# Optimization experiments

Measured on AMD Instinct MI355X. Metric: run time of the kernel, lower is better.

The kernel has to match this reference:

```python
import jax, jax.numpy as jnp
import numpy as np


def setup_inputs() -> dict:
    key = jax.random.key(0)
    kx, kw, kb = jax.random.split(key, 3)
    x = jax.random.normal(kx, (32, 256, 64, 64), dtype=jnp.float32)
    # Conv2d(in=2, out=1, kernel=7) weights, OIHW layout
    W = jax.random.normal(kw, (1, 2, 7, 7), dtype=jnp.float32) * 0.1
    b = jax.random.normal(kb, (1,), dtype=jnp.float32) * 0.1
    return {"x": x, "W": W, "b": b}


def reference(x, W, b):
    # Channel-wise max and mean pooling -> [B, 1, H, W] each
    maxpool = jnp.max(x, axis=1, keepdims=True)
    avgpool = jnp.mean(x, axis=1, keepdims=True)
    pool = jnp.concatenate([maxpool, avgpool], axis=1)  # [B, 2, H, W]
    # 7x7 conv, stride 1, padding 3 (SAME), NCHW / OIHW
    samap = jax.lax.conv_general_dilated(
        pool, W,
        window_strides=(1, 1),
        padding=[(3, 3), (3, 3)],
        dimension_numbers=("NCHW", "OIHW", "NCHW"),
    ) + b[None, :, None, None]
    samap = jax.nn.sigmoid(samap)  # [B, 1, H, W]
    return x * samap
```

## Files before the change

### kernel.cpp

```cpp
#include <hip/hip_runtime.h>
#include <math.h>

constexpr int B_  = 32;
constexpr int C_  = 256;
constexpr int H_  = 64;
constexpr int W_  = 64;
constexpr int HW_ = H_ * W_;
constexpr size_t CHW_ = (size_t)C_ * HW_;

__global__ __launch_bounds__(256) void pool_kernel(const float* __restrict__ x,
                                                   float* __restrict__ pool) {
    const int blk = blockIdx.x;
    const int b   = blk >> 6;
    const int h   = blk & 63;
    const int tid = threadIdx.x;
    const int wg  = tid & 15;
    const int cg  = tid >> 4;

    const float* base = x + (size_t)b * CHW_ + (size_t)(cg * 16) * HW_ + h * W_ + wg * 4;
    float4 v  = *(const float4*)base;
    float4 mx = v, sm = v;
#pragma unroll
    for (int c = 1; c < 16; ++c) {
        float4 u = *(const float4*)(base + (size_t)c * HW_);
        mx.x = fmaxf(mx.x, u.x); mx.y = fmaxf(mx.y, u.y);
        mx.z = fmaxf(mx.z, u.z); mx.w = fmaxf(mx.w, u.w);
        sm.x += u.x; sm.y += u.y; sm.z += u.z; sm.w += u.w;
    }

    __shared__ float4 lmax[16][16];
    __shared__ float4 lsum[16][16];
    lmax[cg][wg] = mx;
    lsum[cg][wg] = sm;
    __syncthreads();

    if (tid < 16) {
        const int w = tid;
        float4 M = lmax[0][w], S = lsum[0][w];
#pragma unroll
        for (int g = 1; g < 16; ++g) {
            float4 m2 = lmax[g][w], s2 = lsum[g][w];
            M.x = fmaxf(M.x, m2.x); M.y = fmaxf(M.y, m2.y);
            M.z = fmaxf(M.z, m2.z); M.w = fmaxf(M.w, m2.w);
            S.x += s2.x; S.y += s2.y; S.z += s2.z; S.w += s2.w;
        }
        const float inv = 1.0f / 256.0f;
        float4 A = make_float4(S.x * inv, S.y * inv, S.z * inv, S.w * inv);
        float* pm = pool + (size_t)b * 2 * HW_ + h * W_ + w * 4;
        *(float4*)pm          = M;
        *(float4*)(pm + HW_)  = A;
    }
}

__global__ __launch_bounds__(256) void conv_kernel(const float* __restrict__ pool,
                                                   const float* __restrict__ Wp,
                                                   const float* __restrict__ bp,
                                                   float* __restrict__ samap) {
    __shared__ float sw[98];
    const int tid = threadIdx.x;
    if (tid < 98) sw[tid] = Wp[tid];
    __syncthreads();

    const int t  = blockIdx.x * 256 + tid;
    const int b  = t >> 12;
    const int hw = t & 4095;
    const int h  = hw >> 6;
    const int w  = hw & 63;

    const float* pb = pool + (size_t)b * 2 * HW_;
    float acc = bp[0];
#pragma unroll
    for (int i = 0; i < 2; ++i) {
        const float* pc = pb + i * HW_;
        const float* wc = sw + i * 49;
#pragma unroll
        for (int kh = 0; kh < 7; ++kh) {
            const int hh = h + kh - 3;
            if (hh < 0 || hh >= H_) continue;
#pragma unroll
            for (int kw = 0; kw < 7; ++kw) {
                const int ww = w + kw - 3;
                if (ww < 0 || ww >= W_) continue;
                acc = fmaf(pc[hh * W_ + ww], wc[kh * 7 + kw], acc);
            }
        }
    }
    samap[t] = 1.0f / (1.0f + expf(-acc));
}

__global__ __launch_bounds__(256) void scale_kernel(const float* __restrict__ x,
                                                    const float* __restrict__ samap,
                                                    float* __restrict__ out) {
    const int t = blockIdx.x * 256 + threadIdx.x;
    const size_t o = (size_t)t * 4;
    const int b  = (int)(o >> 20);
    const int hw = (int)(o & 4095);
    float4 xv = *(const float4*)(x + o);
    float4 sv = *(const float4*)(samap + b * HW_ + hw);
    float4 ov = make_float4(xv.x * sv.x, xv.y * sv.y, xv.z * sv.z, xv.w * sv.w);
    *(float4*)(out + o) = ov;
}

extern "C" void kernel_launch(void* const* d_in, const int* in_sizes, int n_in,
                              void* d_out, int out_size, void* d_ws, size_t ws_size,
                              hipStream_t stream) {
    const float* x  = (const float*)d_in[0];
    const float* Wp = (const float*)d_in[1];
    const float* bp = (const float*)d_in[2];
    float* out = (float*)d_out;

    float* pool  = (float*)d_ws;
    float* samap = pool + (size_t)B_ * 2 * HW_;

    pool_kernel<<<B_ * H_, 256, 0, stream>>>(x, pool);
    conv_kernel<<<(B_ * HW_) / 256, 256, 0, stream>>>(pool, Wp, bp, samap);
    scale_kernel<<<(B_ * (int)CHW_) / (4 * 256), 256, 0, stream>>>(x, samap, out);
}
```

Measured before the change: 264.1 us.

## Fuse conv and scale into one row-wise kernel with nontemporal stores

Merges the 7x7 conv+sigmoid kernel and the broadcast-scale kernel into one kernel per (batch, row). Each block stages the 7 pool rows in shared memory, computes 64 sigmoid values with 64 threads, then scales all 256 channels of that row and writes the output with nontemporal stores. This removes one launch and the samap round trip through global memory. In exchange, 3/4 of the threads sit idle during the conv phase and the block synchronizes before the big streaming phase.

```diff
diff --git a/kernel.cpp b/kernel.cpp
--- a/kernel.cpp
+++ b/kernel.cpp
@@ -7,6 +7,8 @@
 constexpr int W_  = 64;
 constexpr int HW_ = H_ * W_;
 constexpr size_t CHW_ = (size_t)C_ * HW_;
+
+typedef float v4f __attribute__((ext_vector_type(4)));
 
 __global__ __launch_bounds__(256) void pool_kernel(const float* __restrict__ x,
                                                    float* __restrict__ pool) {
@@ -52,53 +54,66 @@
     }
 }
 
-__global__ __launch_bounds__(256) void conv_kernel(const float* __restrict__ pool,
-                                                   const float* __restrict__ Wp,
-                                                   const float* __restrict__ bp,
-                                                   float* __restrict__ samap) {
+__global__ __launch_bounds__(256) void conv_scale_kernel(const float* __restrict__ x,
+                                                         const float* __restrict__ pool,
+                                                         const float* __restrict__ Wp,
+                                                         const float* __restrict__ bp,
+                                                         float* __restrict__ out) {
+    const int blk = blockIdx.x;
+    const int b   = blk >> 6;
+    const int h   = blk & 63;
+    const int tid = threadIdx.x;
+
     __shared__ float sw[98];
-    const int tid = threadIdx.x;
+    __shared__ float spool[2][7][64];
+    __shared__ float ssa[64];
+
     if (tid < 98) sw[tid] = Wp[tid];
+#pragma unroll
+    for (int idx = tid; idx < 896; idx += 256) {
+        const int plane = idx / 448;
+        const int rem   = idx - plane * 448;
+        const int r     = rem >> 6;
+        const int w     = rem & 63;
+        const int hh    = h + r - 3;
+        spool[plane][r][w] = (hh >= 0 && hh < H_)
+            ? pool[((size_t)b * 2 + plane) * HW_ + hh * W_ + w] : 0.0f;
+    }
     __syncthreads();
 
-    const int t  = blockIdx.x * 256 + tid;
-    const int b  = t >> 12;
-    const int hw = t & 4095;
-    const int h  = hw >> 6;
-    const int w  = hw & 63;
-
-    const float* pb = pool + (size_t)b * 2 * HW_;
-    float acc = bp[0];
+    if (tid < 64) {
+        float acc = bp[0];
 #pragma unroll
-    for (int i = 0; i < 2; ++i) {
-        const float* pc = pb + i * HW_;
-        const float* wc = sw + i * 49;
+        for (int p = 0; p < 2; ++p) {
+            const float* wc = sw + p * 49;
 #pragma unroll
-        for (int kh = 0; kh < 7; ++kh) {
-            const int hh = h + kh - 3;
-            if (hh < 0 || hh >= H_) continue;
+            for (int kh = 0; kh < 7; ++kh) {
 #pragma unroll
-            for (int kw = 0; kw < 7; ++kw) {
-                const int ww = w + kw - 3;
-                if (ww < 0 || ww >= W_) continue;
-                acc = fmaf(pc[hh * W_ + ww], wc[kh * 7 + kw], acc);
+                for (int kw = 0; kw < 7; ++kw) {
+                    const int ww = tid + kw - 3;
+                    if (ww >= 0 && ww < W_)
+                        acc = fmaf(spool[p][kh][ww], wc[kh * 7 + kw], acc);
+                }
             }
         }
+        ssa[tid] = 1.0f / (1.0f + expf(-acc));
     }
-    samap[t] = 1.0f / (1.0f + expf(-acc));
-}
+    __syncthreads();
 
-__global__ __launch_bounds__(256) void scale_kernel(const float* __restrict__ x,
-                                                    const float* __restrict__ samap,
-                                                    float* __restrict__ out) {
-    const int t = blockIdx.x * 256 + threadIdx.x;
-    const size_t o = (size_t)t * 4;
-    const int b  = (int)(o >> 20);
-    const int hw = (int)(o & 4095);
-    float4 xv = *(const float4*)(x + o);
-    float4 sv = *(const float4*)(samap + b * HW_ + hw);
-    float4 ov = make_float4(xv.x * sv.x, xv.y * sv.y, xv.z * sv.z, xv.w * sv.w);
-    *(float4*)(out + o) = ov;
+    const int wq = tid & 15;
+    const int c0 = tid >> 4;
+    const float4 sv = *(const float4*)&ssa[wq * 4];
+    const size_t base = (size_t)b * CHW_ + (size_t)c0 * HW_ + h * W_ + wq * 4;
+    const float* xb = x + base;
+    float*       ob = out + base;
+#pragma unroll
+    for (int j = 0; j < 16; ++j) {
+        const float4 xv = *(const float4*)(xb + (size_t)j * 16 * HW_);
+        v4f ov;
+        ov.x = xv.x * sv.x; ov.y = xv.y * sv.y;
+        ov.z = xv.z * sv.z; ov.w = xv.w * sv.w;
+        __builtin_nontemporal_store(ov, (v4f*)(ob + (size_t)j * 16 * HW_));
+    }
 }
 
 extern "C" void kernel_launch(void* const* d_in, const int* in_sizes, int n_in,
@@ -109,10 +124,8 @@
     const float* bp = (const float*)d_in[2];
     float* out = (float*)d_out;
 
-    float* pool  = (float*)d_ws;
-    float* samap = pool + (size_t)B_ * 2 * HW_;
+    float* pool = (float*)d_ws;
 
     pool_kernel<<<B_ * H_, 256, 0, stream>>>(x, pool);
-    conv_kernel<<<(B_ * HW_) / 256, 256, 0, stream>>>(pool, Wp, bp, samap);
-    scale_kernel<<<(B_ * (int)CHW_) / (4 * 256), 256, 0, stream>>>(x, samap, out);
+    conv_scale_kernel<<<B_ * H_, 256, 0, stream>>>(x, pool, Wp, bp, out);
 }
```

Result: faster. 257.8 us (-2.4%).
